# Optimization experiments

Hardware: AMD Instinct MI355X
Metric: run time of the kernel (lower is better)

## Reference

```python
import jax, jax.numpy as jnp
import numpy as np

B, T, N, C_IN, C_OUT, CHEB_K, ST_EMB = 8, 12, 2048, 64, 64, 2, 64


def setup_inputs() -> dict:
    key = jax.random.key(0)
    ks = jax.random.split(key, 9)
    inv = 1.0 / np.sqrt(ST_EMB)
    return {
        "x": jax.random.normal(ks[0], (B, T, N, C_IN), dtype=jnp.float32),
        "adj": jax.random.uniform(ks[1], (N, N), dtype=jnp.float32),
        "st_emb": jax.random.normal(ks[2], (T, 1, ST_EMB), dtype=jnp.float32),
        "weights": jax.random.normal(ks[3], (CHEB_K, C_IN, C_OUT), dtype=jnp.float32) * 0.02,
        "bias": jax.random.normal(ks[4], (C_OUT,), dtype=jnp.float32) * 0.02,
        "W1": jax.random.uniform(ks[5], (ST_EMB, 32), minval=-inv, maxval=inv, dtype=jnp.float32),
        "b1": jax.random.uniform(ks[6], (32,), minval=-inv, maxval=inv, dtype=jnp.float32),
        "W2": jax.random.uniform(ks[7], (32, 1), minval=-1/np.sqrt(32), maxval=1/np.sqrt(32), dtype=jnp.float32),
        "b2": jax.random.uniform(ks[8], (1,), minval=-1/np.sqrt(32), maxval=1/np.sqrt(32), dtype=jnp.float32),
    }


def reference(x, adj, st_emb, weights, bias, W1, b1, W2, b2):
    # lambda MLP: Linear -> ReLU -> Linear, then 1 + relu(.)
    h = jax.nn.relu(st_emb @ W1 + b1)            # [T,1,32]
    lam = 1.0 + jax.nn.relu(h @ W2 + b2)         # [T,1,1]
    c1 = (2.0 * lam - 2.0) / lam                 # [T,1,1] diagonal-scale coefficient
    c2 = 2.0 / lam                               # [T,1,1]
    # identity support einsum == per-time diagonal scaling of x
    x_g1 = c1[None] * x                          # [B,T,N,C]
    # adjacency support: scale factored out of the N x N contraction
    x_g2 = c2[None] * jnp.einsum('nm,btmc->btnc', adj, x)  # [B,T,N,C]
    x_g = jnp.stack([x_g1, x_g2], axis=3)        # [B,T,N,K,C]
    return jnp.einsum('btnki,kio->btno', x_g, weights) + bias
```

## Files before the change

kernel.cpp:

```cpp
#include <hip/hip_runtime.h>
#include <hip/hip_bf16.h>

#define B_ 8
#define T_ 12
#define N_ 2048
#define C_ 64
#define BM 128
#define BK 64

typedef __attribute__((ext_vector_type(4))) float f32x4;
typedef __attribute__((ext_vector_type(4))) __bf16 bf16x4;
typedef __attribute__((ext_vector_type(8))) __bf16 bf16x8;

#define GAS __attribute__((address_space(1)))
#define LAS __attribute__((address_space(3)))

static __device__ __forceinline__ void gld_lds16(const void* g, void* l) {
    __builtin_amdgcn_global_load_lds((const GAS void*)g, (LAS void*)l, 16, 0, 0);
}

#define WS_CBUF 0
#define WS_WTB  1024
#define WS_ADJB 32768
#define WS_P1T  (32768 + 8388608)
#define WS_P0S  (WS_P1T + 25165824)
#define WS_MID  ((size_t)WS_P0S)
#define WS_FULL ((size_t)WS_P0S + 25165824)

__global__ void lam_kernel(const float* __restrict__ st, const float* __restrict__ W1,
                           const float* __restrict__ b1, const float* __restrict__ W2,
                           const float* __restrict__ b2, float* __restrict__ cbuf) {
    const int t = threadIdx.x >> 5;
    const int h = threadIdx.x & 31;
    if (t >= T_) return;
    float acc = b1[h];
    #pragma unroll 8
    for (int e = 0; e < 64; ++e) acc += st[t * 64 + e] * W1[e * 32 + h];
    float hv = fmaxf(acc, 0.f) * W2[h];
    #pragma unroll
    for (int off = 16; off; off >>= 1) hv += __shfl_down(hv, off, 32);
    if (h == 0) {
        float lam = 1.f + fmaxf(hv + b2[0], 0.f);
        cbuf[t]      = 2.f - 2.f / lam;
        cbuf[T_ + t] = 2.f / lam;
    }
}

__global__ void lamw_kernel(const float* __restrict__ st, const float* __restrict__ W1,
                            const float* __restrict__ b1, const float* __restrict__ W2,
                            const float* __restrict__ b2, const float* __restrict__ weights,
                            float* __restrict__ cbuf, __bf16* __restrict__ WtB) {
    const int t = threadIdx.x >> 5;
    const int h = threadIdx.x & 31;
    if (t < T_) {
        float acc = b1[h];
        #pragma unroll 8
        for (int e = 0; e < 64; ++e) acc += st[t * 64 + e] * W1[e * 32 + h];
        float hv = fmaxf(acc, 0.f) * W2[h];
        #pragma unroll
        for (int off = 16; off; off >>= 1) hv += __shfl_down(hv, off, 32);
        if (h == 0) {
            float lam = 1.f + fmaxf(hv + b2[0], 0.f);
            cbuf[t]      = 2.f - 2.f / lam;
            cbuf[T_ + t] = 2.f / lam;
        }
    }
    for (int e = threadIdx.x; e < 64 * 128; e += 512) {
        int o = e >> 7, k = e & 127;
        float v = (k < 64) ? weights[4096 + k * 64 + o] : weights[(k - 64) * 64 + o];
        WtB[o * 128 + k] = (__bf16)v;
    }
}

template<bool FULLP>
__global__ __launch_bounds__(256, 4) void pcvt_kernel(
    const float* __restrict__ x, const float* __restrict__ adj,
    const __bf16* __restrict__ WtB, const float* __restrict__ cbuf,
    const float* __restrict__ bias, __bf16* __restrict__ adjb,
    __bf16* __restrict__ P1T, __bf16* __restrict__ P0S, float* __restrict__ out)
{
    const int bid = blockIdx.x;
    const int tid = threadIdx.x;
    if (bid >= 1536) {
        const size_t i = ((size_t)(bid - 1536) * 256 + tid) * 8;
        const float4 f0 = *(const float4*)&adj[i];
        const float4 f1 = *(const float4*)&adj[i + 4];
        bf16x8 h = { (__bf16)f0.x, (__bf16)f0.y, (__bf16)f0.z, (__bf16)f0.w,
                     (__bf16)f1.x, (__bf16)f1.y, (__bf16)f1.z, (__bf16)f1.w };
        *(bf16x8*)&adjb[i] = h;
        return;
    }
    __shared__ __align__(16) __bf16 T[64 * 128];
    char* TB = (char*)T;
    const int bt = bid >> 4, n0 = (bid & 15) * 128;
    const int l = tid & 63, w = tid >> 6;
    const int lr = l & 15, lk = l >> 4;
    const float c1 = cbuf[bt % T_];

    f32x4 p1[2][4] = {}, p0[2][4] = {};
    #pragma unroll
    for (int ks = 0; ks < 2; ++ks) {
        bf16x8 a[2];
        #pragma unroll
        for (int mi = 0; mi < 2; ++mi) {
            const float* xs = x + ((size_t)bt * N_ + n0 + w * 32 + mi * 16 + lr) * C_ + ks * 32 + lk * 8;
            float4 f0 = *(const float4*)xs;
            float4 f1 = *(const float4*)(xs + 4);
            a[mi] = { (__bf16)f0.x, (__bf16)f0.y, (__bf16)f0.z, (__bf16)f0.w,
                      (__bf16)f1.x, (__bf16)f1.y, (__bf16)f1.z, (__bf16)f1.w };
        }
        #pragma unroll
        for (int nj = 0; nj < 4; ++nj) {
            const __bf16* wb = WtB + (nj * 16 + lr) * 128 + ks * 32 + lk * 8;
            bf16x8 b1v = *(const bf16x8*)wb;
            bf16x8 b0v = *(const bf16x8*)(wb + 64);
            #pragma unroll
            for (int mi = 0; mi < 2; ++mi) {
                p1[mi][nj] = __builtin_amdgcn_mfma_f32_16x16x32_bf16(a[mi], b1v, p1[mi][nj], 0, 0, 0);
                p0[mi][nj] = __builtin_amdgcn_mfma_f32_16x16x32_bf16(a[mi], b0v, p0[mi][nj], 0, 0, 0);
            }
        }
    }
    #pragma unroll
    for (int nj = 0; nj < 4; ++nj) {
        const int o = nj * 16 + lr;
        const float bv = bias[o];
        #pragma unroll
        for (int mi = 0; mi < 2; ++mi)
            #pragma unroll
            for (int q = 0; q < 4; ++q) {
                const int row = w * 32 + mi * 16 + lk * 4 + q;
                const size_t idx = ((size_t)bt * N_ + n0 + row) * C_ + o;
                const float v = c1 * p0[mi][nj][q] + bv;
                if (FULLP) P0S[idx] = (__bf16)v; else out[idx] = v;
            }
    }
    #pragma unroll
    for (int nj = 0; nj < 4; ++nj) {
        const int o = nj * 16 + lr;
        #pragma unroll
        for (int mi = 0; mi < 2; ++mi)
            #pragma unroll
            for (int q = 0; q < 4; ++q) {
                const int row = w * 32 + mi * 16 + lk * 4 + q;
                *(__bf16*)(TB + o * 256 + ((row * 2) ^ ((o & 7) << 4))) = (__bf16)p1[mi][nj][q];
            }
    }
    __syncthreads();
    {
        const int o = tid >> 2, seg = tid & 3;
        __bf16* dst = P1T + ((size_t)bt * 64 + o) * N_ + n0 + seg * 32;
        #pragma unroll
        for (int i = 0; i < 4; ++i) {
            const int chunk = seg * 64 + i * 16;
            *(bf16x8*)(dst + i * 8) = *(const bf16x8*)(TB + o * 256 + (chunk ^ ((o & 7) << 4)));
        }
    }
}

template<bool FULLP>
__global__ __launch_bounds__(256, 2) void dgcn_main4(
    const __bf16* __restrict__ adjb, const __bf16* __restrict__ P1T,
    const __bf16* __restrict__ P0S, const float* __restrict__ cbuf,
    float* __restrict__ out)
{
    __shared__ __align__(16) __bf16 smem[40960];
    char* sb = (char*)smem;

    const int m0  = blockIdx.x * BM;
    const int btg = blockIdx.y;
    const int tid = threadIdx.x;
    const int l   = tid & 63, w = tid >> 6;
    const int wr  = w >> 1, wc = w & 1;
    const int lr  = l & 15, lk = l >> 4;

    const __bf16* srcA[4];
    const __bf16* srcB[6];
    #pragma unroll
    for (int i = 0; i < 4; ++i) {
        int s = (w * 4 + i) * 64 + l;
        int r = s >> 3, j = s & 7;
        srcA[i] = adjb + (size_t)(m0 + r) * N_ + 8 * (j ^ (r & 7));
    }
    #pragma unroll
    for (int i = 0; i < 6; ++i) {
        int s = (w * 6 + i) * 64 + l;
        int btl = s >> 9, rem = s & 511;
        int o = rem >> 3, j = rem & 7;
        srcB[i] = P1T + ((size_t)(btg * 3 + btl) * 64 + o) * N_ + 8 * (j ^ (o & 7));
    }

    f32x4 acc[4][6] = {};

    auto STAGE = [&]__attribute__((always_inline))(int bufsel) {
        const int wo = bufsel * 40960;
        #pragma unroll
        for (int i = 0; i < 4; ++i) {
            gld_lds16(srcA[i], sb + wo + (w * 4 + i) * 1024);
            srcA[i] += BK;
        }
        #pragma unroll
        for (int i = 0; i < 6; ++i) {
            gld_lds16(srcB[i], sb + wo + 16384 + (w * 6 + i) * 1024);
            srcB[i] += BK;
        }
    };

    STAGE(0);
    STAGE(1);

    const int NT = N_ / BK;
    int sel = 0;
    for (int kt = 0; kt < NT; ++kt) {
        if (kt == NT - 1) asm volatile("s_waitcnt vmcnt(0)" ::: "memory");
        else              asm volatile("s_waitcnt vmcnt(10)" ::: "memory");
        __builtin_amdgcn_sched_barrier(0);
        __builtin_amdgcn_s_barrier();

        const char* base = sb + sel * 40960;
        #pragma unroll
        for (int ks = 0; ks < 2; ++ks) {
            const int kb = ks * 64 + lk * 16;
            bf16x8 a[4];
            #pragma unroll
            for (int mi = 0; mi < 4; ++mi) {
                int rr = wr * 64 + mi * 16 + lr;
                a[mi] = *(const bf16x8*)(base + rr * 128 + (kb ^ ((rr & 7) << 4)));
            }
            #pragma unroll
            for (int nj = 0; nj < 6; ++nj) {
                int c = wc * 96 + nj * 16 + lr;
                int btl = c >> 6, o = c & 63;
                bf16x8 b = *(const bf16x8*)(base + 16384 + btl * 8192 + o * 128 + (kb ^ ((o & 7) << 4)));
                #pragma unroll
                for (int mi = 0; mi < 4; ++mi)
                    acc[mi][nj] = __builtin_amdgcn_mfma_f32_16x16x32_bf16(a[mi], b, acc[mi][nj], 0, 0, 0);
            }
        }

        __builtin_amdgcn_s_barrier();
        if (kt + 2 < NT) STAGE(sel);
        sel ^= 1;
    }

    #pragma unroll
    for (int nj = 0; nj < 6; ++nj) {
        const int c = wc * 96 + nj * 16 + lr;
        const int btl = c >> 6, o = c & 63;
        const int btA = btg * 3 + btl;
        const float c2 = cbuf[T_ + (btA % T_)];
        #pragma unroll
        for (int mi = 0; mi < 4; ++mi)
            #pragma unroll
            for (int q = 0; q < 4; ++q) {
                const int row = wr * 64 + mi * 16 + lk * 4 + q;
                const size_t idx = ((size_t)btA * N_ + m0 + row) * C_ + o;
                const float p0v = FULLP ? (float)P0S[idx] : out[idx];
                out[idx] = c2 * acc[mi][nj][q] + p0v;
            }
    }
}

#define LDM 72
#define LDE 136
__global__ __launch_bounds__(256, 3) void dgcn_fb(
    const float* __restrict__ x, const float* __restrict__ adj,
    const float* __restrict__ weights, const float* __restrict__ bias,
    const float* __restrict__ cbuf, float* __restrict__ out)
{
    __shared__ __align__(16) __bf16 smem[BM * LDE];
    __shared__ __align__(16) __bf16 Wt[64 * LDE];
    __bf16* As = smem;
    __bf16* Bs = smem + BM * LDM;
    __bf16* E  = smem;

    const int mtile = blockIdx.x;
    const int bt    = blockIdx.y;
    const int tloc  = bt % T_;
    const int m0    = mtile * BM;
    const int tid   = threadIdx.x;
    const int lane  = tid & 63;
    const int w     = tid >> 6;

    const float c1 = cbuf[tloc];
    const float c2 = cbuf[T_ + tloc];
    const float* xbt = x + (size_t)bt * N_ * C_;

    for (int e = tid; e < 2 * 64 * 64; e += 256) {
        int kk = e >> 6, o = e & 63;
        float v = (kk < 64) ? weights[4096 + kk * 64 + o] : weights[(kk - 64) * 64 + o];
        Wt[o * LDE + kk] = (__bf16)v;
    }

    f32x4 acc[2][4] = {};
    const int c4 = tid & 15;
    const int rg = tid >> 4;
    const int lr = lane & 15;
    const int lk = lane >> 4;

    for (int kt = 0; kt < N_ / BK; ++kt) {
        const int k0 = kt * BK;
        __syncthreads();
        #pragma unroll
        for (int j = 0; j < 8; ++j) {
            const int r = rg + 16 * j;
            const float4 f = *(const float4*)&adj[(size_t)(m0 + r) * N_ + k0 + 4 * c4];
            bf16x4 h = { (__bf16)f.x, (__bf16)f.y, (__bf16)f.z, (__bf16)f.w };
            *(bf16x4*)&As[r * LDM + 4 * c4] = h;
        }
        #pragma unroll
        for (int j = 0; j < 4; ++j) {
            const int k  = (tid & 15) + 16 * j;
            const int c0 = 4 * (tid >> 4);
            const float4 f = *(const float4*)&xbt[(size_t)(k0 + k) * C_ + c0];
            Bs[(c0 + 0) * LDM + k] = (__bf16)f.x;
            Bs[(c0 + 1) * LDM + k] = (__bf16)f.y;
            Bs[(c0 + 2) * LDM + k] = (__bf16)f.z;
            Bs[(c0 + 3) * LDM + k] = (__bf16)f.w;
        }
        __syncthreads();
        #pragma unroll
        for (int ks = 0; ks < 2; ++ks) {
            bf16x8 a0 = *(const bf16x8*)&As[(w * 32 +  0 + lr) * LDM + ks * 32 + lk * 8];
            bf16x8 a1 = *(const bf16x8*)&As[(w * 32 + 16 + lr) * LDM + ks * 32 + lk * 8];
            #pragma unroll
            for (int nj = 0; nj < 4; ++nj) {
                bf16x8 b = *(const bf16x8*)&Bs[(nj * 16 + lr) * LDM + ks * 32 + lk * 8];
                acc[0][nj] = __builtin_amdgcn_mfma_f32_16x16x32_bf16(a0, b, acc[0][nj], 0, 0, 0);
                acc[1][nj] = __builtin_amdgcn_mfma_f32_16x16x32_bf16(a1, b, acc[1][nj], 0, 0, 0);
            }
        }
    }
    __syncthreads();

    #pragma unroll
    for (int j = 0; j < 8; ++j) {
        const int r = rg + 16 * j;
        const float4 f = *(const float4*)&xbt[(size_t)(m0 + r) * C_ + 4 * c4];
        bf16x4 h = { (__bf16)(c1 * f.x), (__bf16)(c1 * f.y), (__bf16)(c1 * f.z), (__bf16)(c1 * f.w) };
        *(bf16x4*)&E[r * LDE + 64 + 4 * c4] = h;
    }
    #pragma unroll
    for (int mi = 0; mi < 2; ++mi)
        #pragma unroll
        for (int nj = 0; nj < 4; ++nj)
            #pragma unroll
            for (int q = 0; q < 4; ++q) {
                const int row = w * 32 + mi * 16 + lk * 4 + q;
                const int col = nj * 16 + lr;
                E[row * LDE + col] = (__bf16)(c2 * acc[mi][nj][q]);
            }
    __syncthreads();

    f32x4 oacc[2][4] = {};
    #pragma unroll
    for (int ks = 0; ks < 4; ++ks) {
        bf16x8 a0 = *(const bf16x8*)&E[(w * 32 +  0 + lr) * LDE + ks * 32 + lk * 8];
        bf16x8 a1 = *(const bf16x8*)&E[(w * 32 + 16 + lr) * LDE + ks * 32 + lk * 8];
        #pragma unroll
        for (int nj = 0; nj < 4; ++nj) {
            bf16x8 bw = *(const bf16x8*)&Wt[(nj * 16 + lr) * LDE + ks * 32 + lk * 8];
            oacc[0][nj] = __builtin_amdgcn_mfma_f32_16x16x32_bf16(a0, bw, oacc[0][nj], 0, 0, 0);
            oacc[1][nj] = __builtin_amdgcn_mfma_f32_16x16x32_bf16(a1, bw, oacc[1][nj], 0, 0, 0);
        }
    }
    float* obt = out + (size_t)bt * N_ * C_;
    #pragma unroll
    for (int nj = 0; nj < 4; ++nj) {
        const float bv = bias[nj * 16 + lr];
        #pragma unroll
        for (int mi = 0; mi < 2; ++mi)
            #pragma unroll
            for (int q = 0; q < 4; ++q) {
                const int row = w * 32 + mi * 16 + lk * 4 + q;
                obt[(size_t)(m0 + row) * C_ + nj * 16 + lr] = oacc[mi][nj][q] + bv;
            }
    }
}

extern "C" void kernel_launch(void* const* d_in, const int* in_sizes, int n_in,
                              void* d_out, int out_size, void* d_ws, size_t ws_size,
                              hipStream_t stream) {
    const float* x       = (const float*)d_in[0];
    const float* adj     = (const float*)d_in[1];
    const float* st_emb  = (const float*)d_in[2];
    const float* weights = (const float*)d_in[3];
    const float* bias    = (const float*)d_in[4];
    const float* W1      = (const float*)d_in[5];
    const float* b1      = (const float*)d_in[6];
    const float* W2      = (const float*)d_in[7];
    const float* b2      = (const float*)d_in[8];
    float* out = (float*)d_out;
    char* ws = (char*)d_ws;
    float* cbuf = (float*)(ws + WS_CBUF);

    if (ws_size >= WS_MID) {
        __bf16* WtB  = (__bf16*)(ws + WS_WTB);
        __bf16* adjb = (__bf16*)(ws + WS_ADJB);
        __bf16* P1T  = (__bf16*)(ws + WS_P1T);
        __bf16* P0S  = (__bf16*)(ws + WS_P0S);
        lamw_kernel<<<1, 512, 0, stream>>>(st_emb, W1, b1, W2, b2, weights, cbuf, WtB);
        if (ws_size >= WS_FULL) {
            pcvt_kernel<true><<<3584, 256, 0, stream>>>(x, adj, WtB, cbuf, bias, adjb, P1T, P0S, out);
            dgcn_main4<true><<<dim3(N_ / BM, 32), 256, 0, stream>>>(adjb, P1T, P0S, cbuf, out);
        } else {
            pcvt_kernel<false><<<3584, 256, 0, stream>>>(x, adj, WtB, cbuf, bias, adjb, P1T, P0S, out);
            dgcn_main4<false><<<dim3(N_ / BM, 32), 256, 0, stream>>>(adjb, P1T, P0S, cbuf, out);
        }
    } else {
        lam_kernel<<<1, 384, 0, stream>>>(st_emb, W1, b1, W2, b2, cbuf);
        dgcn_fb<<<dim3(N_ / BM, B_ * T_), 256, 0, stream>>>(x, adj, weights, bias, cbuf, out);
    }
}
```

Baseline: 93.31 us.

## Load adjacency A-tiles directly into registers, stage only B through LDS

The main GEMM kernel no longer stages the adjacency (A) tile through shared memory. Each wave now loads its own A fragments straight from global memory into registers, double-buffered across two register sets, while only the P1T (B) tile still goes through LDS via async global-to-LDS loads. This cuts LDS footprint and LDS read traffic for A, which could allow more occupancy or fewer bank stalls. In exchange it raises register pressure, and because A rows are shared across the two column-waves, global A loads are duplicated. The A loads also become strided 16-byte per-lane accesses rather than coalesced staged copies.

Result: slower. 127.7 us (+36.9%).

```diff
diff --git a/kernel.cpp b/kernel.cpp
--- a/kernel.cpp
+++ b/kernel.cpp
@@ -159,12 +159,12 @@
 }
 
 template<bool FULLP>
-__global__ __launch_bounds__(256, 2) void dgcn_main4(
+__global__ __launch_bounds__(256, 2) void dgcn_main5(
     const __bf16* __restrict__ adjb, const __bf16* __restrict__ P1T,
     const __bf16* __restrict__ P0S, const float* __restrict__ cbuf,
     float* __restrict__ out)
 {
-    __shared__ __align__(16) __bf16 smem[40960];
+    __shared__ __align__(16) __bf16 smem[24576];
     char* sb = (char*)smem;
 
     const int m0  = blockIdx.x * BM;
@@ -174,14 +174,14 @@
     const int wr  = w >> 1, wc = w & 1;
     const int lr  = l & 15, lk = l >> 4;
 
-    const __bf16* srcA[4];
+    const __bf16* aBase[4][2];
+    #pragma unroll
+    for (int mi = 0; mi < 4; ++mi)
+        #pragma unroll
+        for (int ks = 0; ks < 2; ++ks)
+            aBase[mi][ks] = adjb + (size_t)(m0 + wr * 64 + mi * 16 + lr) * N_ + ks * 32 + lk * 8;
+
     const __bf16* srcB[6];
-    #pragma unroll
-    for (int i = 0; i < 4; ++i) {
-        int s = (w * 4 + i) * 64 + l;
-        int r = s >> 3, j = s & 7;
-        srcA[i] = adjb + (size_t)(m0 + r) * N_ + 8 * (j ^ (r & 7));
-    }
     #pragma unroll
     for (int i = 0; i < 6; ++i) {
         int s = (w * 6 + i) * 64 + l;
@@ -191,56 +191,57 @@
     }
 
     f32x4 acc[4][6] = {};
-
-    auto STAGE = [&]__attribute__((always_inline))(int bufsel) {
-        const int wo = bufsel * 40960;
-        #pragma unroll
-        for (int i = 0; i < 4; ++i) {
-            gld_lds16(srcA[i], sb + wo + (w * 4 + i) * 1024);
-            srcA[i] += BK;
-        }
+    bf16x8 aA[4][2], aB[4][2];
+
+    auto LOADA = [&]__attribute__((always_inline))(bf16x8 (&dst)[4][2]) {
+        #pragma unroll
+        for (int mi = 0; mi < 4; ++mi)
+            #pragma unroll
+            for (int ks = 0; ks < 2; ++ks) {
+                dst[mi][ks] = *(const bf16x8*)aBase[mi][ks];
+                aBase[mi][ks] += BK;
+            }
+    };
+    auto STAGEB = [&]__attribute__((always_inline))(char* buf) {
         #pragma unroll
         for (int i = 0; i < 6; ++i) {
-            gld_lds16(srcB[i], sb + wo + 16384 + (w * 6 + i) * 1024);
+            gld_lds16(srcB[i], buf + (w * 6 + i) * 1024);
             srcB[i] += BK;
         }
     };
-
-    STAGE(0);
-    STAGE(1);
-
-    const int NT = N_ / BK;
-    int sel = 0;
-    for (int kt = 0; kt < NT; ++kt) {
-        if (kt == NT - 1) asm volatile("s_waitcnt vmcnt(0)" ::: "memory");
-        else              asm volatile("s_waitcnt vmcnt(10)" ::: "memory");
-        __builtin_amdgcn_sched_barrier(0);
-        __builtin_amdgcn_s_barrier();
-
-        const char* base = sb + sel * 40960;
+    auto COMPUTE = [&]__attribute__((always_inline))(const char* base, const bf16x8 (&aR)[4][2]) {
         #pragma unroll
         for (int ks = 0; ks < 2; ++ks) {
             const int kb = ks * 64 + lk * 16;
-            bf16x8 a[4];
-            #pragma unroll
-            for (int mi = 0; mi < 4; ++mi) {
-                int rr = wr * 64 + mi * 16 + lr;
-                a[mi] = *(const bf16x8*)(base + rr * 128 + (kb ^ ((rr & 7) << 4)));
-            }
             #pragma unroll
             for (int nj = 0; nj < 6; ++nj) {
                 int c = wc * 96 + nj * 16 + lr;
                 int btl = c >> 6, o = c & 63;
-                bf16x8 b = *(const bf16x8*)(base + 16384 + btl * 8192 + o * 128 + (kb ^ ((o & 7) << 4)));
+                bf16x8 b = *(const bf16x8*)(base + btl * 8192 + o * 128 + (kb ^ ((o & 7) << 4)));
                 #pragma unroll
                 for (int mi = 0; mi < 4; ++mi)
-                    acc[mi][nj] = __builtin_amdgcn_mfma_f32_16x16x32_bf16(a[mi], b, acc[mi][nj], 0, 0, 0);
-            }
-        }
-
+                    acc[mi][nj] = __builtin_amdgcn_mfma_f32_16x16x32_bf16(aR[mi][ks], b, acc[mi][nj], 0, 0, 0);
+            }
+        }
+    };
+
+    const int NT = N_ / BK;
+    auto ITER = [&]__attribute__((always_inline))(int kt, bf16x8 (&aReg)[4][2], char* base) {
+        if (kt == NT - 1) asm volatile("s_waitcnt vmcnt(0)" ::: "memory");
+        else              asm volatile("s_waitcnt vmcnt(14)" ::: "memory");
+        __builtin_amdgcn_sched_barrier(0);
         __builtin_amdgcn_s_barrier();
-        if (kt + 2 < NT) STAGE(sel);
-        sel ^= 1;
+        COMPUTE(base, aReg);
+        __builtin_amdgcn_s_barrier();
+        if (kt + 2 < NT) { LOADA(aReg); STAGEB(base); }
+    };
+
+    LOADA(aA); STAGEB(sb);
+    LOADA(aB); STAGEB(sb + 24576);
+
+    for (int kt = 0; kt < NT; kt += 2) {
+        ITER(kt,     aA, sb);
+        ITER(kt + 1, aB, sb + 24576);
     }
 
     #pragma unroll
@@ -402,10 +403,10 @@
         lamw_kernel<<<1, 512, 0, stream>>>(st_emb, W1, b1, W2, b2, weights, cbuf, WtB);
         if (ws_size >= WS_FULL) {
             pcvt_kernel<true><<<3584, 256, 0, stream>>>(x, adj, WtB, cbuf, bias, adjb, P1T, P0S, out);
-            dgcn_main4<true><<<dim3(N_ / BM, 32), 256, 0, stream>>>(adjb, P1T, P0S, cbuf, out);
+            dgcn_main5<true><<<dim3(N_ / BM, 32), 256, 0, stream>>>(adjb, P1T, P0S, cbuf, out);
         } else {
             pcvt_kernel<false><<<3584, 256, 0, stream>>>(x, adj, WtB, cbuf, bias, adjb, P1T, P0S, out);
-            dgcn_main4<false><<<dim3(N_ / BM, 32), 256, 0, stream>>>(adjb, P1T, P0S, cbuf, out);
+            dgcn_main5<false><<<dim3(N_ / BM, 32), 256, 0, stream>>>(adjb, P1T, P0S, cbuf, out);
         }
     } else {
         lam_kernel<<<1, 384, 0, stream>>>(st_emb, W1, b1, W2, b2, cbuf);
```
